# Performance work log

Hardware: AMD Instinct MI355X
Metric: run time of the kernel (lower is better)

## Reference

```python
import jax, jax.numpy as jnp
import numpy as np

N_NODES = 100000
N_FEAT = 512
HIDDEN = 16
OUT = 2
N_EDGES = 3200000


def gcn_conv(x, edge_index, W, b, n_nodes):
    """PyG-style GCNConv: h = D^-1/2 (A+I) D^-1/2 (x W) + b."""
    h = x @ W  # project first (PyG order) -> [N, out]
    src, dst = edge_index[0], edge_index[1]
    # add self loops
    loop = jnp.arange(n_nodes, dtype=src.dtype)
    src = jnp.concatenate([src, loop])
    dst = jnp.concatenate([dst, loop])
    # symmetric normalization: deg = in-degree (scatter ones to dst)
    deg = jax.ops.segment_sum(jnp.ones_like(dst, dtype=h.dtype), dst, num_segments=n_nodes)
    dinv = jax.lax.rsqrt(deg)  # deg >= 1 due to self loops
    norm = dinv[src] * dinv[dst]  # [E+N]
    msg = h[src] * norm[:, None]  # gather + scale
    out = jax.ops.segment_sum(msg, dst, num_segments=n_nodes)  # scatter-add
    return out + b


def setup_inputs() -> dict:
    key = jax.random.key(0)
    k1, k2, k3, k4, k5 = jax.random.split(key, 5)
    x = jax.random.normal(k1, (N_NODES, N_FEAT), dtype=jnp.float32)
    edge_index = jax.random.randint(k2, (2, N_EDGES), 0, N_NODES, dtype=jnp.int64)
    # Glorot-style params for the two GCNConv layers
    W1 = jax.random.normal(k3, (N_FEAT, HIDDEN), dtype=jnp.float32) / np.sqrt(N_FEAT)
    b1 = jnp.zeros((HIDDEN,), dtype=jnp.float32)
    W2 = jax.random.normal(k4, (HIDDEN, OUT), dtype=jnp.float32) / np.sqrt(HIDDEN)
    b2 = jnp.zeros((OUT,), dtype=jnp.float32)
    return {"x": x, "edge_index": edge_index, "W1": W1, "b1": b1, "W2": W2, "b2": b2}


def reference(x, edge_index, W1, b1, W2, b2):
    n = x.shape[0]
    h = gcn_conv(x, edge_index, W1, b1, n)
    h = jax.nn.relu(h)
    out = gcn_conv(h, edge_index, W2, b2, n)
    return out
```

## Files before the change

### kernel.cpp

```cpp
#include <hip/hip_runtime.h>
#include <hip/hip_fp16.h>

#define NFEAT 512
#define HID 16
#define MAXNB 512
#define NBLK 512
#define PACK_SHIFT 17
#define PACK_MASK ((1 << PACK_SHIFT) - 1)

typedef _Float16 f16x8 __attribute__((ext_vector_type(8)));
typedef float f32x4 __attribute__((ext_vector_type(4)));

__global__ __launch_bounds__(512) void k_hist2d(const int* __restrict__ ei,
                                                int* __restrict__ cnt_t,
                                                int E, int nb) {
  __shared__ int l[MAXNB];
  for (int i = threadIdx.x; i < nb; i += 512) l[i] = 0;
  __syncthreads();
  int chunk = (E + NBLK - 1) / NBLK;
  int beg = blockIdx.x * chunk;
  int end = beg + chunk; if (end > E) end = E;
  for (int e = beg + threadIdx.x; e < end; e += 512)
    atomicAdd(&l[ei[(size_t)E + e] >> 8], 1);
  __syncthreads();
  for (int b = threadIdx.x; b < nb; b += 512)
    cnt_t[(size_t)b * NBLK + blockIdx.x] = l[b];
}

__global__ __launch_bounds__(64) void k_colscan(const int* __restrict__ cnt_t,
                                                int* __restrict__ off_t,
                                                int* __restrict__ gcnt, int nb) {
  int b = blockIdx.x;
  if (b >= nb) return;
  int lane = threadIdx.x;
  int4 v0 = *(const int4*)&cnt_t[(size_t)b * NBLK + lane * 8];
  int4 v1 = *(const int4*)&cnt_t[(size_t)b * NBLK + lane * 8 + 4];
  int tot = (v0.x + v0.y + v0.z + v0.w) + (v1.x + v1.y + v1.z + v1.w);
  int s = tot;
  for (int d = 1; d < 64; d <<= 1) {
    int o = __shfl_up(s, d);
    if (lane >= d) s += o;
  }
  int excl = s - tot;
  int4 w0, w1;
  w0.x = excl;
  w0.y = w0.x + v0.x;
  w0.z = w0.y + v0.y;
  w0.w = w0.z + v0.z;
  w1.x = w0.w + v0.w;
  w1.y = w1.x + v1.x;
  w1.z = w1.y + v1.y;
  w1.w = w1.z + v1.z;
  *(int4*)&off_t[(size_t)b * NBLK + lane * 8] = w0;
  *(int4*)&off_t[(size_t)b * NBLK + lane * 8 + 4] = w1;
  if (lane == 63) gcnt[b] = s;
}

__global__ __launch_bounds__(512) void k_bscan(const int* __restrict__ gcnt,
                                               int* __restrict__ gbase, int nb) {
  __shared__ int sm[512];
  int t = threadIdx.x;
  int c = (t < nb) ? gcnt[t] : 0;
  int pc = (c + 15) & ~15;
  sm[t] = pc;
  __syncthreads();
  for (int off = 1; off < 512; off <<= 1) {
    int x = (t >= off) ? sm[t - off] : 0;
    __syncthreads();
    sm[t] += x;
    __syncthreads();
  }
  if (t < nb) gbase[t] = sm[t] - pc;
}

__global__ __launch_bounds__(512) void k_scatter2(const int* __restrict__ ei,
                                                  const int* __restrict__ gbase,
                                                  const int* __restrict__ off_t,
                                                  int* __restrict__ binned,
                                                  int E, int nb) {
  __shared__ int cur[MAXNB];
  for (int b = threadIdx.x; b < nb; b += 512)
    cur[b] = gbase[b] + off_t[(size_t)b * NBLK + blockIdx.x];
  __syncthreads();
  int chunk = (E + NBLK - 1) / NBLK;
  int beg = blockIdx.x * chunk;
  int end = beg + chunk; if (end > E) end = E;
  for (int e = beg + threadIdx.x; e < end; e += 512) {
    int s = ei[e];
    int d = ei[(size_t)E + e];
    int b = d >> 8;
    int pos = atomicAdd(&cur[b], 1);
    binned[pos] = s | ((d & 255) << PACK_SHIFT);
  }
}

__global__ __launch_bounds__(512) void k_sortbucket(const int* __restrict__ gbase,
                                                    const int* __restrict__ gcnt,
                                                    const int* __restrict__ binned,
                                                    int* __restrict__ csr,
                                                    int* __restrict__ rowbeg,
                                                    int* __restrict__ rowend,
                                                    float* __restrict__ dinv, int N) {
  __shared__ int hist[256];
  __shared__ int sm[256];
  __shared__ int cur[256];
  const int t = threadIdx.x;
  const int b = blockIdx.x;
  const int base = gbase[b], cnt = gcnt[b];
  if (t < 256) hist[t] = 0;
  __syncthreads();
  for (int j = base + t; j < base + cnt; j += 512)
    atomicAdd(&hist[binned[j] >> PACK_SHIFT], 1);
  __syncthreads();
  int h = 0;
  if (t < 256) {
    h = hist[t];
    sm[t] = h;
  }
  __syncthreads();
  for (int off = 1; off < 256; off <<= 1) {
    int x = 0;
    if (t < 256 && t >= off) x = sm[t - off];
    __syncthreads();
    if (t < 256) sm[t] += x;
    __syncthreads();
  }
  if (t < 256) {
    int incl = sm[t];
    int excl = incl - h;
    cur[t] = excl;
    int node = b * 256 + t;
    if (node < N) {
      rowbeg[node] = base + excl;
      rowend[node] = base + incl;
      dinv[node] = rsqrtf((float)h + 1.0f);
    }
  }
  __syncthreads();
  for (int j = base + t; j < base + cnt; j += 512) {
    int val = binned[j];
    int pos = atomicAdd(&cur[val >> PACK_SHIFT], 1);
    csr[base + pos] = val & PACK_MASK;
  }
}

__global__ __launch_bounds__(256) void k_gemm1(const float* __restrict__ x,
                                               const float* __restrict__ W,
                                               const float* __restrict__ dinv,
                                               __half* __restrict__ h1h, int N) {
  const int wid = threadIdx.x >> 6;
  const int lane = threadIdx.x & 63;
  const int n = lane & 15;
  const int g = lane >> 4;

  const int ntiles = (N + 15) >> 4;
  const int tile = blockIdx.x * 4 + wid;
  if (tile >= ntiles) return;

  f16x8 bf[16];
#pragma unroll
  for (int f = 0; f < 16; ++f) {
    const float* wp = W + (size_t)(f * 32 + g * 8) * HID + n;
#pragma unroll
    for (int j = 0; j < 8; ++j) bf[f][j] = (_Float16)wp[j * HID];
  }

  int rowbase = tile * 16;
  if (rowbase + 16 > N) rowbase = N - 16;
  const float* xr = x + (size_t)(rowbase + n) * NFEAT + g * 8;

  f32x4 acc = {0.f, 0.f, 0.f, 0.f};
#pragma unroll
  for (int f = 0; f < 16; ++f) {
    float4 p0 = *(const float4*)(xr + f * 32);
    float4 p1 = *(const float4*)(xr + f * 32 + 4);
    f16x8 af;
    af[0] = (_Float16)p0.x; af[1] = (_Float16)p0.y;
    af[2] = (_Float16)p0.z; af[3] = (_Float16)p0.w;
    af[4] = (_Float16)p1.x; af[5] = (_Float16)p1.y;
    af[6] = (_Float16)p1.z; af[7] = (_Float16)p1.w;
    acc = __builtin_amdgcn_mfma_f32_16x16x32_f16(af, bf[f], acc, 0, 0, 0);
  }

#pragma unroll
  for (int r = 0; r < 4; ++r) {
    int row = rowbase + g * 4 + r;
    h1h[(size_t)row * HID + n] = __float2half(acc[r] * dinv[row]);
  }
}

__global__ __launch_bounds__(256) void k_agg1f(const int* __restrict__ rowbeg,
                                               const int* __restrict__ rowend,
                                               const int* __restrict__ csr,
                                               const __half* __restrict__ h1h,
                                               const float* __restrict__ dinv,
                                               const float* __restrict__ b1,
                                               const float* __restrict__ W2,
                                               float* __restrict__ h2s, int N) {
  const int f = threadIdx.x & 15;
  const int node = blockIdx.x * 16 + (threadIdx.x >> 4);
  if (node >= N) return;
  int j = rowbeg[node];
  const int end = rowend[node];
  float acc = __half2float(h1h[(size_t)node * HID + f]);
  for (; j < end && (j & 3); ++j) acc += __half2float(h1h[(size_t)csr[j] * HID + f]);
  for (; j + 8 <= end; j += 8) {
    int4 s0 = *(const int4*)&csr[j];
    int4 s1 = *(const int4*)&csr[j + 4];
    float a0 = __half2float(h1h[(size_t)s0.x * HID + f]);
    float a1 = __half2float(h1h[(size_t)s0.y * HID + f]);
    float a2 = __half2float(h1h[(size_t)s0.z * HID + f]);
    float a3 = __half2float(h1h[(size_t)s0.w * HID + f]);
    float a4 = __half2float(h1h[(size_t)s1.x * HID + f]);
    float a5 = __half2float(h1h[(size_t)s1.y * HID + f]);
    float a6 = __half2float(h1h[(size_t)s1.z * HID + f]);
    float a7 = __half2float(h1h[(size_t)s1.w * HID + f]);
    acc += ((a0 + a1) + (a2 + a3)) + ((a4 + a5) + (a6 + a7));
  }
  for (; j + 4 <= end; j += 4) {
    int4 ss = *(const int4*)&csr[j];
    float a0 = __half2float(h1h[(size_t)ss.x * HID + f]);
    float a1 = __half2float(h1h[(size_t)ss.y * HID + f]);
    float a2 = __half2float(h1h[(size_t)ss.z * HID + f]);
    float a3 = __half2float(h1h[(size_t)ss.w * HID + f]);
    acc += (a0 + a1) + (a2 + a3);
  }
  for (; j < end; ++j) acc += __half2float(h1h[(size_t)csr[j] * HID + f]);

  float di = dinv[node];
  float v = fmaxf(acc * di + b1[f], 0.f);
  float o0 = v * W2[f * 2 + 0];
  float o1 = v * W2[f * 2 + 1];
#pragma unroll
  for (int d = 1; d < 16; d <<= 1) {
    o0 += __shfl_xor(o0, d);
    o1 += __shfl_xor(o1, d);
  }
  if (f == 0) *(float2*)&h2s[(size_t)node * 2] = make_float2(o0 * di, o1 * di);
}

__global__ __launch_bounds__(256) void k_agg2f(const int* __restrict__ rowbeg,
                                               const int* __restrict__ rowend,
                                               const int* __restrict__ csr,
                                               const float* __restrict__ h2s,
                                               const float* __restrict__ dinv,
                                               const float* __restrict__ b2,
                                               float* __restrict__ out, int N) {
  int i = blockIdx.x * 256 + threadIdx.x;
  if (i >= N) return;
  int j = rowbeg[i];
  const int end = rowend[i];
  float2 o = *(const float2*)&h2s[(size_t)i * 2];
  for (; j < end && (j & 3); ++j) {
    float2 v = *(const float2*)&h2s[(size_t)csr[j] * 2];
    o.x += v.x; o.y += v.y;
  }
  for (; j + 4 <= end; j += 4) {
    int4 ss = *(const int4*)&csr[j];
    float2 v0 = *(const float2*)&h2s[(size_t)ss.x * 2];
    float2 v1 = *(const float2*)&h2s[(size_t)ss.y * 2];
    float2 v2 = *(const float2*)&h2s[(size_t)ss.z * 2];
    float2 v3 = *(const float2*)&h2s[(size_t)ss.w * 2];
    o.x += (v0.x + v1.x) + (v2.x + v3.x);
    o.y += (v0.y + v1.y) + (v2.y + v3.y);
  }
  for (; j < end; ++j) {
    float2 v = *(const float2*)&h2s[(size_t)csr[j] * 2];
    o.x += v.x; o.y += v.y;
  }
  float di = dinv[i];
  o.x = o.x * di + b2[0];
  o.y = o.y * di + b2[1];
  *(float2*)&out[(size_t)i * 2] = o;
}

extern "C" void kernel_launch(void* const* d_in, const int* in_sizes, int n_in,
                              void* d_out, int out_size, void* d_ws, size_t ws_size,
                              hipStream_t stream) {
  const float* x = (const float*)d_in[0];
  const int* ei = (const int*)d_in[1];
  const float* W1 = (const float*)d_in[2];
  const float* b1 = (const float*)d_in[3];
  const float* W2 = (const float*)d_in[4];
  const float* b2 = (const float*)d_in[5];
  float* out = (float*)d_out;
  const int N = in_sizes[0] / NFEAT;
  const int E = in_sizes[1] / 2;
  const int nb = (N + 255) / 256;

  char* p = (char*)d_ws;
  int* cnt_t = (int*)p;    p += (size_t)MAXNB * NBLK * 4;
  int* off_t = (int*)p;    p += (size_t)MAXNB * NBLK * 4;
  int* gcnt = (int*)p;     p += (size_t)MAXNB * 4;
  int* gbase = (int*)p;    p += (size_t)MAXNB * 4;
  int* binned = (int*)p;   p += ((size_t)E + MAXNB * 16) * 4;
  int* csr = (int*)p;      p += ((size_t)E + MAXNB * 16) * 4;
  int* rowbeg = (int*)p;   p += (size_t)N * 4;
  int* rowend = (int*)p;   p += (size_t)N * 4;
  float* dinv = (float*)p; p += (size_t)N * 4;
  __half* h1h = (__half*)p; p += (size_t)N * HID * 2;
  float* h2s = (float*)p;  p += (size_t)N * 2 * 4;

  const int ntiles = (N + 15) / 16;
  const int gblocks = (ntiles + 3) / 4;

  k_hist2d<<<NBLK, 512, 0, stream>>>(ei, cnt_t, E, nb);
  k_colscan<<<nb, 64, 0, stream>>>(cnt_t, off_t, gcnt, nb);
  k_bscan<<<1, 512, 0, stream>>>(gcnt, gbase, nb);
  k_scatter2<<<NBLK, 512, 0, stream>>>(ei, gbase, off_t, binned, E, nb);
  k_sortbucket<<<nb, 512, 0, stream>>>(gbase, gcnt, binned, csr, rowbeg, rowend, dinv, N);
  k_gemm1<<<gblocks, 256, 0, stream>>>(x, W1, dinv, h1h, N);
  k_agg1f<<<(N + 15) / 16, 256, 0, stream>>>(rowbeg, rowend, csr, h1h, dinv, b1, W2, h2s, N);
  k_agg2f<<<(N + 255) / 256, 256, 0, stream>>>(rowbeg, rowend, csr, h2s, dinv, b2, out, N);
}
```

Baseline: 167.4 us.

## Overlap dense GEMM with edge histogram and scatter kernels, defer dinv scaling

The standalone x@W1 GEMM is split in half, and each half runs as extra blocks inside the histogram and scatter kernels. The memory-bound edge passes and the x read can then share the GPU. Because dinv is not known when the GEMM runs, the GEMM writes unscaled fp16 results, and the bucket-sort kernel rescales each node's row by its dinv afterwards. The layer-2 aggregation also gains an 8-wide unrolled gather loop. In exchange, the large blocks are heterogeneous and h1 takes an extra read-modify-write pass.

Result: no change. 166.3 us (-0.7%).

```diff
diff --git a/kernel.cpp b/kernel.cpp
--- a/kernel.cpp
+++ b/kernel.cpp
@@ -11,20 +11,68 @@
 typedef _Float16 f16x8 __attribute__((ext_vector_type(8)));
 typedef float f32x4 __attribute__((ext_vector_type(4)));
 
-__global__ __launch_bounds__(512) void k_hist2d(const int* __restrict__ ei,
-                                                int* __restrict__ cnt_t,
-                                                int E, int nb) {
+__device__ __forceinline__ void gemm_tile(const float* __restrict__ x,
+                                          const float* __restrict__ W,
+                                          __half* __restrict__ h1u,
+                                          int tile, int N, int lane) {
+  const int n = lane & 15;
+  const int g = lane >> 4;
+
+  f16x8 bf[16];
+#pragma unroll
+  for (int f = 0; f < 16; ++f) {
+    const float* wp = W + (size_t)(f * 32 + g * 8) * HID + n;
+#pragma unroll
+    for (int j = 0; j < 8; ++j) bf[f][j] = (_Float16)wp[j * HID];
+  }
+
+  int rowbase = tile * 16;
+  if (rowbase + 16 > N) rowbase = N - 16;
+  const float* xr = x + (size_t)(rowbase + n) * NFEAT + g * 8;
+
+  f32x4 acc = {0.f, 0.f, 0.f, 0.f};
+#pragma unroll
+  for (int f = 0; f < 16; ++f) {
+    float4 p0 = *(const float4*)(xr + f * 32);
+    float4 p1 = *(const float4*)(xr + f * 32 + 4);
+    f16x8 af;
+    af[0] = (_Float16)p0.x; af[1] = (_Float16)p0.y;
+    af[2] = (_Float16)p0.z; af[3] = (_Float16)p0.w;
+    af[4] = (_Float16)p1.x; af[5] = (_Float16)p1.y;
+    af[6] = (_Float16)p1.z; af[7] = (_Float16)p1.w;
+    acc = __builtin_amdgcn_mfma_f32_16x16x32_f16(af, bf[f], acc, 0, 0, 0);
+  }
+
+#pragma unroll
+  for (int r = 0; r < 4; ++r) {
+    int row = rowbase + g * 4 + r;
+    h1u[(size_t)row * HID + n] = __float2half(acc[r]);
+  }
+}
+
+__global__ __launch_bounds__(512) void k_hist_gemm(const int* __restrict__ ei,
+                                                   int* __restrict__ cnt_t,
+                                                   int E, int nb,
+                                                   const float* __restrict__ x,
+                                                   const float* __restrict__ W,
+                                                   __half* __restrict__ h1u,
+                                                   int N, int tsplit) {
   __shared__ int l[MAXNB];
-  for (int i = threadIdx.x; i < nb; i += 512) l[i] = 0;
-  __syncthreads();
-  int chunk = (E + NBLK - 1) / NBLK;
-  int beg = blockIdx.x * chunk;
-  int end = beg + chunk; if (end > E) end = E;
-  for (int e = beg + threadIdx.x; e < end; e += 512)
-    atomicAdd(&l[ei[(size_t)E + e] >> 8], 1);
-  __syncthreads();
-  for (int b = threadIdx.x; b < nb; b += 512)
-    cnt_t[(size_t)b * NBLK + blockIdx.x] = l[b];
+  if (blockIdx.x < NBLK) {
+    for (int i = threadIdx.x; i < nb; i += 512) l[i] = 0;
+    __syncthreads();
+    int chunk = (E + NBLK - 1) / NBLK;
+    int beg = blockIdx.x * chunk;
+    int end = beg + chunk; if (end > E) end = E;
+    for (int e = beg + threadIdx.x; e < end; e += 512)
+      atomicAdd(&l[ei[(size_t)E + e] >> 8], 1);
+    __syncthreads();
+    for (int b = threadIdx.x; b < nb; b += 512)
+      cnt_t[(size_t)b * NBLK + blockIdx.x] = l[b];
+  } else {
+    int tile = (blockIdx.x - NBLK) * 8 + (threadIdx.x >> 6);
+    if (tile < tsplit) gemm_tile(x, W, h1u, tile, N, threadIdx.x & 63);
+  }
 }
 
 __global__ __launch_bounds__(64) void k_colscan(const int* __restrict__ cnt_t,
@@ -73,24 +121,33 @@
   if (t < nb) gbase[t] = sm[t] - pc;
 }
 
-__global__ __launch_bounds__(512) void k_scatter2(const int* __restrict__ ei,
-                                                  const int* __restrict__ gbase,
-                                                  const int* __restrict__ off_t,
-                                                  int* __restrict__ binned,
-                                                  int E, int nb) {
+__global__ __launch_bounds__(512) void k_scatter_gemm(const int* __restrict__ ei,
+                                                      const int* __restrict__ gbase,
+                                                      const int* __restrict__ off_t,
+                                                      int* __restrict__ binned,
+                                                      int E, int nb,
+                                                      const float* __restrict__ x,
+                                                      const float* __restrict__ W,
+                                                      __half* __restrict__ h1u,
+                                                      int N, int tsplit, int ntiles) {
   __shared__ int cur[MAXNB];
-  for (int b = threadIdx.x; b < nb; b += 512)
-    cur[b] = gbase[b] + off_t[(size_t)b * NBLK + blockIdx.x];
-  __syncthreads();
-  int chunk = (E + NBLK - 1) / NBLK;
-  int beg = blockIdx.x * chunk;
-  int end = beg + chunk; if (end > E) end = E;
-  for (int e = beg + threadIdx.x; e < end; e += 512) {
-    int s = ei[e];
-    int d = ei[(size_t)E + e];
-    int b = d >> 8;
-    int pos = atomicAdd(&cur[b], 1);
-    binned[pos] = s | ((d & 255) << PACK_SHIFT);
+  if (blockIdx.x < NBLK) {
+    for (int b = threadIdx.x; b < nb; b += 512)
+      cur[b] = gbase[b] + off_t[(size_t)b * NBLK + blockIdx.x];
+    __syncthreads();
+    int chunk = (E + NBLK - 1) / NBLK;
+    int beg = blockIdx.x * chunk;
+    int end = beg + chunk; if (end > E) end = E;
+    for (int e = beg + threadIdx.x; e < end; e += 512) {
+      int s = ei[e];
+      int d = ei[(size_t)E + e];
+      int b = d >> 8;
+      int pos = atomicAdd(&cur[b], 1);
+      binned[pos] = s | ((d & 255) << PACK_SHIFT);
+    }
+  } else {
+    int tile = tsplit + (blockIdx.x - NBLK) * 8 + (threadIdx.x >> 6);
+    if (tile < ntiles) gemm_tile(x, W, h1u, tile, N, threadIdx.x & 63);
   }
 }
 
@@ -100,10 +157,12 @@
                                                     int* __restrict__ csr,
                                                     int* __restrict__ rowbeg,
                                                     int* __restrict__ rowend,
-                                                    float* __restrict__ dinv, int N) {
+                                                    float* __restrict__ dinv,
+                                                    __half* __restrict__ h1h, int N) {
   __shared__ int hist[256];
   __shared__ int sm[256];
   __shared__ int cur[256];
+  __shared__ float sdinv[256];
   const int t = threadIdx.x;
   const int b = blockIdx.x;
   const int base = gbase[b], cnt = gcnt[b];
@@ -129,11 +188,13 @@
     int incl = sm[t];
     int excl = incl - h;
     cur[t] = excl;
+    float dv = rsqrtf((float)h + 1.0f);
+    sdinv[t] = dv;
     int node = b * 256 + t;
     if (node < N) {
       rowbeg[node] = base + excl;
       rowend[node] = base + incl;
-      dinv[node] = rsqrtf((float)h + 1.0f);
+      dinv[node] = dv;
     }
   }
   __syncthreads();
@@ -142,50 +203,16 @@
     int pos = atomicAdd(&cur[val >> PACK_SHIFT], 1);
     csr[base + pos] = val & PACK_MASK;
   }
-}
-
-__global__ __launch_bounds__(256) void k_gemm1(const float* __restrict__ x,
-                                               const float* __restrict__ W,
-                                               const float* __restrict__ dinv,
-                                               __half* __restrict__ h1h, int N) {
-  const int wid = threadIdx.x >> 6;
-  const int lane = threadIdx.x & 63;
-  const int n = lane & 15;
-  const int g = lane >> 4;
-
-  const int ntiles = (N + 15) >> 4;
-  const int tile = blockIdx.x * 4 + wid;
-  if (tile >= ntiles) return;
-
-  f16x8 bf[16];
-#pragma unroll
-  for (int f = 0; f < 16; ++f) {
-    const float* wp = W + (size_t)(f * 32 + g * 8) * HID + n;
-#pragma unroll
-    for (int j = 0; j < 8; ++j) bf[f][j] = (_Float16)wp[j * HID];
-  }
-
-  int rowbase = tile * 16;
-  if (rowbase + 16 > N) rowbase = N - 16;
-  const float* xr = x + (size_t)(rowbase + n) * NFEAT + g * 8;
-
-  f32x4 acc = {0.f, 0.f, 0.f, 0.f};
-#pragma unroll
-  for (int f = 0; f < 16; ++f) {
-    float4 p0 = *(const float4*)(xr + f * 32);
-    float4 p1 = *(const float4*)(xr + f * 32 + 4);
-    f16x8 af;
-    af[0] = (_Float16)p0.x; af[1] = (_Float16)p0.y;
-    af[2] = (_Float16)p0.z; af[3] = (_Float16)p0.w;
-    af[4] = (_Float16)p1.x; af[5] = (_Float16)p1.y;
-    af[6] = (_Float16)p1.z; af[7] = (_Float16)p1.w;
-    acc = __builtin_amdgcn_mfma_f32_16x16x32_f16(af, bf[f], acc, 0, 0, 0);
-  }
-
-#pragma unroll
-  for (int r = 0; r < 4; ++r) {
-    int row = rowbase + g * 4 + r;
-    h1h[(size_t)row * HID + n] = __float2half(acc[r] * dinv[row]);
+  {
+    int node = b * 256 + (t >> 1);
+    if (node < N) {
+      float dv = sdinv[t >> 1];
+      __half* hp = h1h + (size_t)node * HID + (t & 1) * 8;
+      f16x8 v = *(const f16x8*)hp;
+#pragma unroll
+      for (int j = 0; j < 8; ++j) v[j] = (_Float16)((float)v[j] * dv);
+      *(f16x8*)hp = v;
+    }
   }
 }
 
@@ -255,6 +282,20 @@
     float2 v = *(const float2*)&h2s[(size_t)csr[j] * 2];
     o.x += v.x; o.y += v.y;
   }
+  for (; j + 8 <= end; j += 8) {
+    int4 s0 = *(const int4*)&csr[j];
+    int4 s1 = *(const int4*)&csr[j + 4];
+    float2 v0 = *(const float2*)&h2s[(size_t)s0.x * 2];
+    float2 v1 = *(const float2*)&h2s[(size_t)s0.y * 2];
+    float2 v2 = *(const float2*)&h2s[(size_t)s0.z * 2];
+    float2 v3 = *(const float2*)&h2s[(size_t)s0.w * 2];
+    float2 v4 = *(const float2*)&h2s[(size_t)s1.x * 2];
+    float2 v5 = *(const float2*)&h2s[(size_t)s1.y * 2];
+    float2 v6 = *(const float2*)&h2s[(size_t)s1.z * 2];
+    float2 v7 = *(const float2*)&h2s[(size_t)s1.w * 2];
+    o.x += ((v0.x + v1.x) + (v2.x + v3.x)) + ((v4.x + v5.x) + (v6.x + v7.x));
+    o.y += ((v0.y + v1.y) + (v2.y + v3.y)) + ((v4.y + v5.y) + (v6.y + v7.y));
+  }
   for (; j + 4 <= end; j += 4) {
     int4 ss = *(const int4*)&csr[j];
     float2 v0 = *(const float2*)&h2s[(size_t)ss.x * 2];
@@ -302,14 +343,17 @@
   float* h2s = (float*)p;  p += (size_t)N * 2 * 4;
 
   const int ntiles = (N + 15) / 16;
-  const int gblocks = (ntiles + 3) / 4;
-
-  k_hist2d<<<NBLK, 512, 0, stream>>>(ei, cnt_t, E, nb);
+  const int tsplit = ((ntiles / 2) + 7) & ~7;
+  const int gA = (tsplit + 7) / 8;
+  const int gB = (ntiles - tsplit + 7) / 8;
+
+  k_hist_gemm<<<NBLK + gA, 512, 0, stream>>>(ei, cnt_t, E, nb, x, W1, h1h, N, tsplit);
   k_colscan<<<nb, 64, 0, stream>>>(cnt_t, off_t, gcnt, nb);
   k_bscan<<<1, 512, 0, stream>>>(gcnt, gbase, nb);
-  k_scatter2<<<NBLK, 512, 0, stream>>>(ei, gbase, off_t, binned, E, nb);
-  k_sortbucket<<<nb, 512, 0, stream>>>(gbase, gcnt, binned, csr, rowbeg, rowend, dinv, N);
-  k_gemm1<<<gblocks, 256, 0, stream>>>(x, W1, dinv, h1h, N);
+  k_scatter_gemm<<<NBLK + gB, 512, 0, stream>>>(ei, gbase, off_t, binned, E, nb,
+                                                x, W1, h1h, N, tsplit, ntiles);
+  k_sortbucket<<<nb, 512, 0, stream>>>(gbase, gcnt, binned, csr, rowbeg, rowend,
+                                       dinv, h1h, N);
   k_agg1f<<<(N + 15) / 16, 256, 0, stream>>>(rowbeg, rowend, csr, h1h, dinv, b1, W2, h2s, N);
   k_agg2f<<<(N + 255) / 256, 256, 0, stream>>>(rowbeg, rowend, csr, h2s, dinv, b2, out, N);
 }
```
